# Performance work log

Measured on AMD Instinct MI355X. Metric: run time of the kernel, lower is better.

The kernel has to match this reference:

```python
import jax, jax.numpy as jnp
import numpy as np

B, S, D, H = 2, 2048, 1024, 16
HD = D // H  # head_dim = 64


def setup_inputs() -> dict:
    key = jax.random.key(0)
    ks = jax.random.split(key, 9)
    scale = 0.02
    x = jax.random.normal(ks[0], (B, S, D), dtype=jnp.float32)
    wq = jax.random.normal(ks[1], (D, D), dtype=jnp.float32) * scale
    bq = jnp.zeros((D,), dtype=jnp.float32)
    wk = jax.random.normal(ks[2], (D, D), dtype=jnp.float32) * scale
    bk = jnp.zeros((D,), dtype=jnp.float32)
    wv = jax.random.normal(ks[3], (D, D), dtype=jnp.float32) * scale
    bv = jnp.zeros((D,), dtype=jnp.float32)
    wo = jax.random.normal(ks[4], (D, D), dtype=jnp.float32) * scale
    bo = jnp.zeros((D,), dtype=jnp.float32)
    # causal mask: 1.0 where key position is in the future of query position
    mask = jnp.triu(jnp.ones((S, S), dtype=jnp.float32), k=1)[None, None]  # [1,1,S,S]
    return {"x": x, "wq": wq, "bq": bq, "wk": wk, "bk": bk,
            "wv": wv, "bv": bv, "wo": wo, "bo": bo, "mask": mask}


def reference(x, wq, bq, wk, bk, wv, bv, wo, bo, mask):
    b, s, d = x.shape
    q = (x @ wq + bq).reshape(b, s, H, HD).transpose(0, 2, 1, 3)  # [b,h,s,hd]
    k = (x @ wk + bk).reshape(b, s, H, HD).transpose(0, 2, 1, 3)
    v = (x @ wv + bv).reshape(b, s, H, HD).transpose(0, 2, 1, 3)
    scores = jnp.einsum('bhqd,bhkd->bhqk', q, k) / jnp.sqrt(jnp.float32(HD))
    scores = scores + mask * (-1e9)
    probs = jax.nn.softmax(scores, axis=-1)
    out = jnp.einsum('bhqk,bhkd->bhqd', probs, v)
    out = out.transpose(0, 2, 1, 3).reshape(b, s, d)
    return out @ wo + bo
```

## Files before the change

### kernel.cpp

```cpp
#include <hip/hip_runtime.h>
#include <hip/hip_bf16.h>
#include <cstdint>

#define DEV static __device__ __forceinline__

typedef unsigned short u16t;
typedef __attribute__((ext_vector_type(4))) float f32x4;
typedef __attribute__((ext_vector_type(4))) unsigned short u16x4;
typedef __attribute__((ext_vector_type(8))) unsigned short u16x8;
typedef __attribute__((ext_vector_type(8))) __bf16 bf16x8;

DEV u16t f2bf(float f) {
  unsigned u = __builtin_bit_cast(unsigned, f);
  u += 0x7fffu + ((u >> 16) & 1u);
  return (u16t)(u >> 16);
}
DEV float bf2f(u16t h) {
  unsigned u = ((unsigned)h) << 16;
  return __builtin_bit_cast(float, u);
}

DEV void gload_lds16(const void* g, void* l) {
  __builtin_amdgcn_global_load_lds(
      (const __attribute__((address_space(1))) void*)g,
      (__attribute__((address_space(3))) void*)l, 16, 0, 0);
}

DEV bf16x8 ldsfrag(const u16t* p) {
  return __builtin_bit_cast(bf16x8, *(const u16x8*)p);
}

DEV void bsync() {
  asm volatile("" ::: "memory");
  __builtin_amdgcn_s_barrier();
  asm volatile("" ::: "memory");
}

__global__ __launch_bounds__(256) void k_convert_x(const float* __restrict__ x,
                                                   u16t* __restrict__ xb) {
  int i = (blockIdx.x * 256 + threadIdx.x) * 4;
  f32x4 v = *(const f32x4*)&x[i];
  u16x4 o;
#pragma unroll
  for (int j = 0; j < 4; ++j) o[j] = f2bf(v[j]);
  *(u16x4*)&xb[i] = o;
}

__global__ __launch_bounds__(256) void k_transw(const float* __restrict__ w0,
                                                const float* __restrict__ w1,
                                                const float* __restrict__ w2,
                                                const float* __restrict__ w3,
                                                u16t* __restrict__ qkvT,
                                                u16t* __restrict__ oT) {
  __shared__ float lds[64][68];
  int z = blockIdx.z;
  const float* W = (z == 0) ? w0 : (z == 1) ? w1 : (z == 2) ? w2 : w3;
  u16t* OUT = (z < 3) ? (qkvT + (size_t)z * 1024 * 1024) : oT;
  int k0 = blockIdx.x * 64, n0 = blockIdx.y * 64;
  int t = threadIdx.x;
  int kl = t >> 4, n4 = (t & 15) << 2;
#pragma unroll
  for (int p = 0; p < 4; ++p) {
    f32x4 v = *(const f32x4*)&W[(size_t)(k0 + kl + p * 16) * 1024 + n0 + n4];
    *(f32x4*)&lds[kl + p * 16][n4] = v;
  }
  __syncthreads();
  int nl = t >> 4, k4 = (t & 15) << 2;
#pragma unroll
  for (int p = 0; p < 4; ++p) {
    int n = nl + p * 16;
    u16x4 o;
#pragma unroll
    for (int i = 0; i < 4; ++i) o[i] = f2bf(lds[k4 + i][n]);
    *(u16x4*)&OUT[(size_t)(n0 + n) * 1024 + k0 + k4] = o;
  }
}

template <bool BF16_OUT, bool VSPLIT>
__global__ __launch_bounds__(256) void k_gemm_bt(const u16t* __restrict__ A,
                                                 const u16t* __restrict__ BT,
                                                 void* __restrict__ Cout,
                                                 const float* __restrict__ b0,
                                                 const float* __restrict__ b1,
                                                 const float* __restrict__ b2,
                                                 u16t* __restrict__ vt,
                                                 int M, int N, int K) {
  __shared__ u16t Al[2][128 * 64];
  __shared__ u16t Bl[2][128 * 64];
  const int tid = threadIdx.x;
  const int l = tid & 63;
  const int w = tid >> 6;
  const int m0 = blockIdx.x * 128, n0 = blockIdx.y * 128;
  const int wm = (w >> 1) * 64, wn = (w & 1) * 64;
  const int lm = l & 15, lh = l >> 4;
  f32x4 acc[4][4] = {};

  auto stage = [&](int bb, int t) {
    const int k0 = t << 6;
#pragma unroll
    for (int s = 0; s < 4; ++s) {
      int c = s * 256 + tid;
      int row = c >> 3, slot = c & 7;
      int ks = k0 + (((slot ^ (row & 7)) & 7) << 3);
      gload_lds16(A + (size_t)(m0 + row) * K + ks, &Al[bb][c * 8]);
    }
#pragma unroll
    for (int s = 0; s < 4; ++s) {
      int c = s * 256 + tid;
      int row = c >> 3, slot = c & 7;
      int ks = k0 + (((slot ^ (row & 7)) & 7) << 3);
      gload_lds16(BT + (size_t)(n0 + row) * K + ks, &Bl[bb][c * 8]);
    }
  };

  const int nt = K >> 6;
  stage(0, 0);
  for (int t = 0; t < nt; ++t) {
    if (t + 1 < nt) {
      stage((t + 1) & 1, t + 1);
      asm volatile("s_waitcnt vmcnt(8)" ::: "memory");
    } else {
      asm volatile("s_waitcnt vmcnt(0)" ::: "memory");
    }
    bsync();
    const int buf = t & 1;

#pragma unroll
    for (int kk = 0; kk < 2; ++kk) {
      bf16x8 af[4], bfr[4];
#pragma unroll
      for (int i = 0; i < 4; ++i) {
        int ra = wm + i * 16 + lm;
        int sa = (kk * 4 + lh) ^ (ra & 7);
        af[i] = ldsfrag(&Al[buf][ra * 64 + sa * 8]);
        int rb = wn + i * 16 + lm;
        int sb = (kk * 4 + lh) ^ (rb & 7);
        bfr[i] = ldsfrag(&Bl[buf][rb * 64 + sb * 8]);
      }
#pragma unroll
      for (int i = 0; i < 4; ++i)
#pragma unroll
        for (int j = 0; j < 4; ++j)
          acc[i][j] = __builtin_amdgcn_mfma_f32_16x16x32_bf16(af[i], bfr[j],
                                                              acc[i][j], 0, 0, 0);
    }
    bsync();
  }

  if (!VSPLIT || (n0 + wn) < 2048) {
#pragma unroll
    for (int i = 0; i < 4; ++i) {
      int row = m0 + wm + i * 16 + (lh << 2);
#pragma unroll
      for (int j = 0; j < 4; ++j) {
        int col = n0 + wn + j * 16 + lm;
        const float* bp = (col < 1024) ? b0 : ((col < 2048) ? b1 : b2);
        float bias = bp[col & 1023];
#pragma unroll
        for (int r = 0; r < 4; ++r) {
          float v = acc[i][j][r] + bias;
          if (BF16_OUT)
            ((u16t*)Cout)[(size_t)(row + r) * N + col] = f2bf(v);
          else
            ((float*)Cout)[(size_t)(row + r) * N + col] = v;
        }
      }
    }
  } else {
#pragma unroll
    for (int i = 0; i < 4; ++i) {
      int row = m0 + wm + i * 16 + (lh << 2);
      int bidx = row >> 11, s0 = row & 2047;
#pragma unroll
    for (int j = 0; j < 4; ++j) {
        int col = n0 + wn + j * 16 + lm;
        int d = col - 2048;
        int hh = d >> 6, dd = d & 63;
        float bias = b2[d];
        u16x4 o;
#pragma unroll
        for (int r = 0; r < 4; ++r) o[r] = f2bf(acc[i][j][r] + bias);
        *(u16x4*)&vt[((size_t)((bidx * 16 + hh) * 64 + dd)) * 2048 + s0] = o;
      }
    }
  }
}

__global__ __launch_bounds__(256, 2) void k_attn(const u16t* __restrict__ qkv,
                                                 const u16t* __restrict__ vt,
                                                 u16t* __restrict__ outp) {
  __shared__ u16t Kl[2][4096];
  __shared__ u16t Vl[2][4096];
  __shared__ u16t Pl[4][2][1024];
  __shared__ u16t pad[4096];
  const int tid = threadIdx.x, l = tid & 63, w = tid >> 6;
  const int lm = l & 15, lh = l >> 4;
  const int bh = blockIdx.x, b = bh >> 4, h = bh & 15;
  const int y = blockIdx.y;
  const int qt = (y < 8) ? y : (23 - y);
  const int q0 = qt * 128;
  const int nt = 2 * qt + 2;
  const int qbase = q0 + w * 32;
  if ((size_t)qkv == 1) pad[tid] = 0;

  const u16t* Kg = qkv + (size_t)b * 2048 * 3072 + 1024 + h * 64;
  const u16t* Vg = vt + (size_t)bh * 64 * 2048;

  bf16x8 aq[2][2];
#pragma unroll
  for (int qm = 0; qm < 2; ++qm)
#pragma unroll
    for (int kk = 0; kk < 2; ++kk) {
      const u16t* src = qkv + (size_t)(b * 2048 + qbase + qm * 16 + lm) * 3072 +
                        h * 64 + kk * 32 + lh * 8;
      u16x8 v = *(const u16x8*)src;
      u16x8 o;
#pragma unroll
      for (int e = 0; e < 8; ++e) o[e] = f2bf(bf2f(v[e]) * 0.125f);
      aq[qm][kk] = __builtin_bit_cast(bf16x8, o);
    }

  float mrun[2] = {-1e30f, -1e30f};
  float lsum[2] = {0.f, 0.f};
  f32x4 aco[2][4] = {};
  const int qr0 = qbase + lm, qr1 = qbase + 16 + lm;

  auto stage = [&](int bb, int t) {
#pragma unroll
    for (int s = 0; s < 2; ++s) {
      int c = s * 256 + tid;
      int row = c >> 3, col = ((c & 7) ^ (row & 7)) << 3;
      gload_lds16(Kg + (size_t)(t * 64 + row) * 3072 + col, &Kl[bb][c * 8]);
    }
#pragma unroll
    for (int s = 0; s < 2; ++s) {
      int c = s * 256 + tid;
      int row = c >> 3, col = ((c & 7) ^ (row & 7)) << 3;
      gload_lds16(Vg + (size_t)row * 2048 + t * 64 + col, &Vl[bb][c * 8]);
    }
  };

  stage(0, 0);

  int buf = 0;
  for (int t = 0; t < nt; ++t) {
    if (t + 1 < nt) {
      stage(buf ^ 1, t + 1);
      asm volatile("s_waitcnt vmcnt(4)" ::: "memory");
    } else {
      asm volatile("s_waitcnt vmcnt(0)" ::: "memory");
    }
    bsync();

    if (t * 64 <= qbase + 31) {
      f32x4 accs[2][4] = {};
#pragma unroll
      for (int kk = 0; kk < 2; ++kk) {
        bf16x8 ak[4];
#pragma unroll
        for (int nk = 0; nk < 4; ++nk) {
          int rk = nk * 16 + lm;
          int s16 = (kk * 4 + lh) ^ (rk & 7);
          ak[nk] = ldsfrag(&Kl[buf][rk * 64 + s16 * 8]);
        }
        __builtin_amdgcn_s_setprio(1);
#pragma unroll
        for (int nk = 0; nk < 4; ++nk) {
          accs[0][nk] = __builtin_amdgcn_mfma_f32_16x16x32_bf16(
              ak[nk], aq[0][kk], accs[0][nk], 0, 0, 0);
          accs[1][nk] = __builtin_amdgcn_mfma_f32_16x16x32_bf16(
              ak[nk], aq[1][kk], accs[1][nk], 0, 0, 0);
        }
        __builtin_amdgcn_s_setprio(0);
      }

      float vmax[2] = {-1e30f, -1e30f};
      if (t * 64 + 63 > qbase) {
#pragma unroll
        for (int nk = 0; nk < 4; ++nk)
#pragma unroll
          for (int r = 0; r < 4; ++r) {
            int kvpos = t * 64 + nk * 16 + lh * 4 + r;
            float v0 = accs[0][nk][r];
            v0 = (kvpos > qr0) ? -1e30f : v0;
            accs[0][nk][r] = v0;
            vmax[0] = fmaxf(vmax[0], v0);
            float v1 = accs[1][nk][r];
            v1 = (kvpos > qr1) ? -1e30f : v1;
            accs[1][nk][r] = v1;
            vmax[1] = fmaxf(vmax[1], v1);
          }
      } else {
#pragma unroll
        for (int nk = 0; nk < 4; ++nk)
#pragma unroll
          for (int r = 0; r < 4; ++r) {
            vmax[0] = fmaxf(vmax[0], accs[0][nk][r]);
            vmax[1] = fmaxf(vmax[1], accs[1][nk][r]);
          }
      }

      if (!__all((vmax[0] <= mrun[0] + 8.f) & (vmax[1] <= mrun[1] + 8.f))) {
#pragma unroll
        for (int qm = 0; qm < 2; ++qm) {
          float rm = fmaxf(vmax[qm], __shfl_xor(vmax[qm], 16));
          rm = fmaxf(rm, __shfl_xor(rm, 32));
          float mnew = fmaxf(mrun[qm], rm);
          float alpha = __expf(mrun[qm] - mnew);
          mrun[qm] = mnew;
          lsum[qm] *= alpha;
#pragma unroll
          for (int r = 0; r < 4; ++r) {
            float ar = __shfl(alpha, lh * 4 + r);
#pragma unroll
            for (int nd = 0; nd < 4; ++nd) aco[qm][nd][r] *= ar;
          }
        }
      }

#pragma unroll
      for (int qm = 0; qm < 2; ++qm) {
        u16t* Pw = &Pl[w][qm][0];
#pragma unroll
        for (int nk = 0; nk < 4; ++nk) {
          float p0 = __expf(accs[qm][nk][0] - mrun[qm]);
          float p1 = __expf(accs[qm][nk][1] - mrun[qm]);
          float p2 = __expf(accs[qm][nk][2] - mrun[qm]);
          float p3 = __expf(accs[qm][nk][3] - mrun[qm]);
          lsum[qm] += (p0 + p1) + (p2 + p3);
          unsigned wlo, whi;
          asm("v_cvt_pk_bf16_f32 %0, %1, %2" : "=v"(wlo) : "v"(p0), "v"(p1));
          asm("v_cvt_pk_bf16_f32 %0, %1, %2" : "=v"(whi) : "v"(p2), "v"(p3));
          int off = lm * 64 + ((((2 * nk + (lh >> 1)) ^ (lm & 7)) & 7) << 3) +
                    ((lh & 1) << 2);
          *(uint2*)&Pw[off] = make_uint2(wlo, whi);
        }
      }

#pragma unroll
      for (int kk = 0; kk < 2; ++kk) {
        int sp = (kk * 4 + lh) ^ (lm & 7);
        bf16x8 ap0 = ldsfrag(&Pl[w][0][lm * 64 + sp * 8]);
        bf16x8 ap1 = ldsfrag(&Pl[w][1][lm * 64 + sp * 8]);
        __builtin_amdgcn_s_setprio(1);
#pragma unroll
        for (int nd = 0; nd < 4; ++nd) {
          int rv = nd * 16 + lm;
          int sv = (kk * 4 + lh) ^ (rv & 7);
          bf16x8 bv = ldsfrag(&Vl[buf][rv * 64 + sv * 8]);
          aco[0][nd] =
              __builtin_amdgcn_mfma_f32_16x16x32_bf16(ap0, bv, aco[0][nd], 0, 0, 0);
          aco[1][nd] =
              __builtin_amdgcn_mfma_f32_16x16x32_bf16(ap1, bv, aco[1][nd], 0, 0, 0);
        }
        __builtin_amdgcn_s_setprio(0);
      }
    }

    bsync();
    buf ^= 1;
  }

#pragma unroll
  for (int qm = 0; qm < 2; ++qm) {
    float ls = lsum[qm];
    ls += __shfl_xor(ls, 16);
    ls += __shfl_xor(ls, 32);
    float inv = 1.0f / ls;
#pragma unroll
    for (int r = 0; r < 4; ++r) {
      float ir = __shfl(inv, lh * 4 + r);
      int row = q0 + w * 32 + qm * 16 + lh * 4 + r;
#pragma unroll
      for (int nd = 0; nd < 4; ++nd) {
        int col = h * 64 + nd * 16 + lm;
        outp[(size_t)(b * 2048 + row) * 1024 + col] = f2bf(aco[qm][nd][r] * ir);
      }
    }
  }
}

extern "C" void kernel_launch(void* const* d_in, const int* in_sizes, int n_in,
                              void* d_out, int out_size, void* d_ws, size_t ws_size,
                              hipStream_t stream) {
  const float* x = (const float*)d_in[0];
  const float* wq = (const float*)d_in[1];
  const float* bq = (const float*)d_in[2];
  const float* wk = (const float*)d_in[3];
  const float* bk = (const float*)d_in[4];
  const float* wv = (const float*)d_in[5];
  const float* bv = (const float*)d_in[6];
  const float* wo = (const float*)d_in[7];
  const float* bo = (const float*)d_in[8];

  char* ws = (char*)d_ws;
  u16t* xb = (u16t*)ws;
  u16t* wqkvT = (u16t*)(ws + (8u << 20));
  u16t* woT = (u16t*)(ws + (14u << 20));
  u16t* qkv = (u16t*)(ws + (16u << 20));
  u16t* vt = (u16t*)(ws + (40u << 20));
  u16t* attn_out = xb;

  k_convert_x<<<4096, 256, 0, stream>>>(x, xb);
  k_transw<<<dim3(16, 16, 4), 256, 0, stream>>>(wq, wk, wv, wo, wqkvT, woT);
  k_gemm_bt<true, true><<<dim3(32, 24), 256, 0, stream>>>(xb, wqkvT, qkv, bq, bk,
                                                          bv, vt, 4096, 3072, 1024);
  k_attn<<<dim3(32, 16), 256, 0, stream>>>(qkv, vt, attn_out);
  k_gemm_bt<false, false><<<dim3(32, 8), 256, 0, stream>>>(
      attn_out, woT, d_out, bo, bo, bo, nullptr, 4096, 1024, 1024);
}
```

Measured before the change: 121.3 us.

## Shrink attention blocks to 64 query rows with 2 waves and exp2 softmax

Attention blocks now cover 64 query rows with two waves instead of 128 rows with four, which doubles the grid to 1024 blocks. The q-tile order is reshuffled to balance the causal workload across the grid. Because each block now only processes full or diagonal KV tiles, the per-wave skip check is removed and the mask is applied only on the last tile. The LDS padding array that limited occupancy is dropped, and the softmax switches to exp2 with log2(e) folded into the Q prescale. In exchange, each KV tile loaded into LDS is reused by fewer query rows, so total K/V traffic roughly doubles.

```diff
diff --git a/kernel.cpp b/kernel.cpp
--- a/kernel.cpp
+++ b/kernel.cpp
@@ -186,22 +186,20 @@
   }
 }
 
-__global__ __launch_bounds__(256, 2) void k_attn(const u16t* __restrict__ qkv,
+__global__ __launch_bounds__(128, 2) void k_attn(const u16t* __restrict__ qkv,
                                                  const u16t* __restrict__ vt,
                                                  u16t* __restrict__ outp) {
   __shared__ u16t Kl[2][4096];
   __shared__ u16t Vl[2][4096];
-  __shared__ u16t Pl[4][2][1024];
-  __shared__ u16t pad[4096];
+  __shared__ u16t Pl[2][2][1024];
   const int tid = threadIdx.x, l = tid & 63, w = tid >> 6;
   const int lm = l & 15, lh = l >> 4;
   const int bh = blockIdx.x, b = bh >> 4, h = bh & 15;
   const int y = blockIdx.y;
-  const int qt = (y < 8) ? y : (23 - y);
-  const int q0 = qt * 128;
-  const int nt = 2 * qt + 2;
+  const int qt = (y < 8) ? y : (y < 16) ? (39 - y) : (y < 24) ? (y - 8) : (47 - y);
+  const int q0 = qt * 64;
+  const int nt = qt + 1;
   const int qbase = q0 + w * 32;
-  if ((size_t)qkv == 1) pad[tid] = 0;
 
   const u16t* Kg = qkv + (size_t)b * 2048 * 3072 + 1024 + h * 64;
   const u16t* Vg = vt + (size_t)bh * 64 * 2048;
@@ -216,7 +214,7 @@
       u16x8 v = *(const u16x8*)src;
       u16x8 o;
 #pragma unroll
-      for (int e = 0; e < 8; ++e) o[e] = f2bf(bf2f(v[e]) * 0.125f);
+      for (int e = 0; e < 8; ++e) o[e] = f2bf(bf2f(v[e]) * 0.1803368801f);
       aq[qm][kk] = __builtin_bit_cast(bf16x8, o);
     }
 
@@ -227,14 +225,14 @@
 
   auto stage = [&](int bb, int t) {
 #pragma unroll
-    for (int s = 0; s < 2; ++s) {
-      int c = s * 256 + tid;
+    for (int s = 0; s < 4; ++s) {
+      int c = s * 128 + tid;
       int row = c >> 3, col = ((c & 7) ^ (row & 7)) << 3;
       gload_lds16(Kg + (size_t)(t * 64 + row) * 3072 + col, &Kl[bb][c * 8]);
     }
 #pragma unroll
-    for (int s = 0; s < 2; ++s) {
-      int c = s * 256 + tid;
+    for (int s = 0; s < 4; ++s) {
+      int c = s * 128 + tid;
       int row = c >> 3, col = ((c & 7) ^ (row & 7)) << 3;
       gload_lds16(Vg + (size_t)row * 2048 + t * 64 + col, &Vl[bb][c * 8]);
     }
@@ -246,115 +244,113 @@
   for (int t = 0; t < nt; ++t) {
     if (t + 1 < nt) {
       stage(buf ^ 1, t + 1);
-      asm volatile("s_waitcnt vmcnt(4)" ::: "memory");
+      asm volatile("s_waitcnt vmcnt(8)" ::: "memory");
     } else {
       asm volatile("s_waitcnt vmcnt(0)" ::: "memory");
     }
     bsync();
 
-    if (t * 64 <= qbase + 31) {
-      f32x4 accs[2][4] = {};
-#pragma unroll
-      for (int kk = 0; kk < 2; ++kk) {
-        bf16x8 ak[4];
-#pragma unroll
-        for (int nk = 0; nk < 4; ++nk) {
-          int rk = nk * 16 + lm;
-          int s16 = (kk * 4 + lh) ^ (rk & 7);
-          ak[nk] = ldsfrag(&Kl[buf][rk * 64 + s16 * 8]);
+    f32x4 accs[2][4] = {};
+#pragma unroll
+    for (int kk = 0; kk < 2; ++kk) {
+      bf16x8 ak[4];
+#pragma unroll
+      for (int nk = 0; nk < 4; ++nk) {
+        int rk = nk * 16 + lm;
+        int s16 = (kk * 4 + lh) ^ (rk & 7);
+        ak[nk] = ldsfrag(&Kl[buf][rk * 64 + s16 * 8]);
+      }
+      __builtin_amdgcn_s_setprio(1);
+#pragma unroll
+      for (int nk = 0; nk < 4; ++nk) {
+        accs[0][nk] = __builtin_amdgcn_mfma_f32_16x16x32_bf16(ak[nk], aq[0][kk],
+                                                              accs[0][nk], 0, 0, 0);
+        accs[1][nk] = __builtin_amdgcn_mfma_f32_16x16x32_bf16(ak[nk], aq[1][kk],
+                                                              accs[1][nk], 0, 0, 0);
+      }
+      __builtin_amdgcn_s_setprio(0);
+    }
+
+    float vmax[2] = {-1e30f, -1e30f};
+    if (t == nt - 1) {
+#pragma unroll
+      for (int nk = 0; nk < 4; ++nk)
+#pragma unroll
+        for (int r = 0; r < 4; ++r) {
+          int kvpos = t * 64 + nk * 16 + lh * 4 + r;
+          float v0 = accs[0][nk][r];
+          v0 = (kvpos > qr0) ? -1e30f : v0;
+          accs[0][nk][r] = v0;
+          vmax[0] = fmaxf(vmax[0], v0);
+          float v1 = accs[1][nk][r];
+          v1 = (kvpos > qr1) ? -1e30f : v1;
+          accs[1][nk][r] = v1;
+          vmax[1] = fmaxf(vmax[1], v1);
         }
-        __builtin_amdgcn_s_setprio(1);
-#pragma unroll
-        for (int nk = 0; nk < 4; ++nk) {
-          accs[0][nk] = __builtin_amdgcn_mfma_f32_16x16x32_bf16(
-              ak[nk], aq[0][kk], accs[0][nk], 0, 0, 0);
-          accs[1][nk] = __builtin_amdgcn_mfma_f32_16x16x32_bf16(
-              ak[nk], aq[1][kk], accs[1][nk], 0, 0, 0);
+    } else {
+#pragma unroll
+      for (int nk = 0; nk < 4; ++nk)
+#pragma unroll
+        for (int r = 0; r < 4; ++r) {
+          vmax[0] = fmaxf(vmax[0], accs[0][nk][r]);
+          vmax[1] = fmaxf(vmax[1], accs[1][nk][r]);
         }
-        __builtin_amdgcn_s_setprio(0);
-      }
-
-      float vmax[2] = {-1e30f, -1e30f};
-      if (t * 64 + 63 > qbase) {
-#pragma unroll
-        for (int nk = 0; nk < 4; ++nk)
-#pragma unroll
-          for (int r = 0; r < 4; ++r) {
-            int kvpos = t * 64 + nk * 16 + lh * 4 + r;
-            float v0 = accs[0][nk][r];
-            v0 = (kvpos > qr0) ? -1e30f : v0;
-            accs[0][nk][r] = v0;
-            vmax[0] = fmaxf(vmax[0], v0);
-            float v1 = accs[1][nk][r];
-            v1 = (kvpos > qr1) ? -1e30f : v1;
-            accs[1][nk][r] = v1;
-            vmax[1] = fmaxf(vmax[1], v1);
-          }
-      } else {
-#pragma unroll
-        for (int nk = 0; nk < 4; ++nk)
-#pragma unroll
-          for (int r = 0; r < 4; ++r) {
-            vmax[0] = fmaxf(vmax[0], accs[0][nk][r]);
-            vmax[1] = fmaxf(vmax[1], accs[1][nk][r]);
-          }
-      }
-
-      if (!__all((vmax[0] <= mrun[0] + 8.f) & (vmax[1] <= mrun[1] + 8.f))) {
-#pragma unroll
-        for (int qm = 0; qm < 2; ++qm) {
-          float rm = fmaxf(vmax[qm], __shfl_xor(vmax[qm], 16));
-          rm = fmaxf(rm, __shfl_xor(rm, 32));
-          float mnew = fmaxf(mrun[qm], rm);
-          float alpha = __expf(mrun[qm] - mnew);
-          mrun[qm] = mnew;
-          lsum[qm] *= alpha;
-#pragma unroll
-          for (int r = 0; r < 4; ++r) {
-            float ar = __shfl(alpha, lh * 4 + r);
-#pragma unroll
-            for (int nd = 0; nd < 4; ++nd) aco[qm][nd][r] *= ar;
-          }
+    }
+
+    if (!__all((vmax[0] <= mrun[0] + 8.f) & (vmax[1] <= mrun[1] + 8.f))) {
+#pragma unroll
+      for (int qm = 0; qm < 2; ++qm) {
+        float rm = fmaxf(vmax[qm], __shfl_xor(vmax[qm], 16));
+        rm = fmaxf(rm, __shfl_xor(rm, 32));
+        float mnew = fmaxf(mrun[qm], rm);
+        float alpha = exp2f(mrun[qm] - mnew);
+        mrun[qm] = mnew;
+        lsum[qm] *= alpha;
+#pragma unroll
+        for (int r = 0; r < 4; ++r) {
+          float ar = __shfl(alpha, lh * 4 + r);
+#pragma unroll
+          for (int nd = 0; nd < 4; ++nd) aco[qm][nd][r] *= ar;
         }
       }
-
-#pragma unroll
-      for (int qm = 0; qm < 2; ++qm) {
-        u16t* Pw = &Pl[w][qm][0];
-#pragma unroll
-        for (int nk = 0; nk < 4; ++nk) {
-          float p0 = __expf(accs[qm][nk][0] - mrun[qm]);
-          float p1 = __expf(accs[qm][nk][1] - mrun[qm]);
-          float p2 = __expf(accs[qm][nk][2] - mrun[qm]);
-          float p3 = __expf(accs[qm][nk][3] - mrun[qm]);
-          lsum[qm] += (p0 + p1) + (p2 + p3);
-          unsigned wlo, whi;
-          asm("v_cvt_pk_bf16_f32 %0, %1, %2" : "=v"(wlo) : "v"(p0), "v"(p1));
-          asm("v_cvt_pk_bf16_f32 %0, %1, %2" : "=v"(whi) : "v"(p2), "v"(p3));
-          int off = lm * 64 + ((((2 * nk + (lh >> 1)) ^ (lm & 7)) & 7) << 3) +
-                    ((lh & 1) << 2);
-          *(uint2*)&Pw[off] = make_uint2(wlo, whi);
-        }
-      }
-
-#pragma unroll
-      for (int kk = 0; kk < 2; ++kk) {
-        int sp = (kk * 4 + lh) ^ (lm & 7);
-        bf16x8 ap0 = ldsfrag(&Pl[w][0][lm * 64 + sp * 8]);
-        bf16x8 ap1 = ldsfrag(&Pl[w][1][lm * 64 + sp * 8]);
-        __builtin_amdgcn_s_setprio(1);
-#pragma unroll
-        for (int nd = 0; nd < 4; ++nd) {
-          int rv = nd * 16 + lm;
-          int sv = (kk * 4 + lh) ^ (rv & 7);
-          bf16x8 bv = ldsfrag(&Vl[buf][rv * 64 + sv * 8]);
-          aco[0][nd] =
-              __builtin_amdgcn_mfma_f32_16x16x32_bf16(ap0, bv, aco[0][nd], 0, 0, 0);
-          aco[1][nd] =
-              __builtin_amdgcn_mfma_f32_16x16x32_bf16(ap1, bv, aco[1][nd], 0, 0, 0);
-        }
-        __builtin_amdgcn_s_setprio(0);
-      }
+    }
+
+#pragma unroll
+    for (int qm = 0; qm < 2; ++qm) {
+      u16t* Pw = &Pl[w][qm][0];
+#pragma unroll
+      for (int nk = 0; nk < 4; ++nk) {
+        float p0 = exp2f(accs[qm][nk][0] - mrun[qm]);
+        float p1 = exp2f(accs[qm][nk][1] - mrun[qm]);
+        float p2 = exp2f(accs[qm][nk][2] - mrun[qm]);
+        float p3 = exp2f(accs[qm][nk][3] - mrun[qm]);
+        lsum[qm] += (p0 + p1) + (p2 + p3);
+        unsigned wlo, whi;
+        asm("v_cvt_pk_bf16_f32 %0, %1, %2" : "=v"(wlo) : "v"(p0), "v"(p1));
+        asm("v_cvt_pk_bf16_f32 %0, %1, %2" : "=v"(whi) : "v"(p2), "v"(p3));
+        int off = lm * 64 + ((((2 * nk + (lh >> 1)) ^ (lm & 7)) & 7) << 3) +
+                  ((lh & 1) << 2);
+        *(uint2*)&Pw[off] = make_uint2(wlo, whi);
+      }
+    }
+
+#pragma unroll
+    for (int kk = 0; kk < 2; ++kk) {
+      int sp = (kk * 4 + lh) ^ (lm & 7);
+      bf16x8 ap0 = ldsfrag(&Pl[w][0][lm * 64 + sp * 8]);
+      bf16x8 ap1 = ldsfrag(&Pl[w][1][lm * 64 + sp * 8]);
+      __builtin_amdgcn_s_setprio(1);
+#pragma unroll
+      for (int nd = 0; nd < 4; ++nd) {
+        int rv = nd * 16 + lm;
+        int sv = (kk * 4 + lh) ^ (rv & 7);
+        bf16x8 bv = ldsfrag(&Vl[buf][rv * 64 + sv * 8]);
+        aco[0][nd] =
+            __builtin_amdgcn_mfma_f32_16x16x32_bf16(ap0, bv, aco[0][nd], 0, 0, 0);
+        aco[1][nd] =
+            __builtin_amdgcn_mfma_f32_16x16x32_bf16(ap1, bv, aco[1][nd], 0, 0, 0);
+      }
+      __builtin_amdgcn_s_setprio(0);
     }
 
     bsync();
@@ -370,7 +366,7 @@
 #pragma unroll
     for (int r = 0; r < 4; ++r) {
       float ir = __shfl(inv, lh * 4 + r);
-      int row = q0 + w * 32 + qm * 16 + lh * 4 + r;
+      int row = qbase + qm * 16 + lh * 4 + r;
 #pragma unroll
       for (int nd = 0; nd < 4; ++nd) {
         int col = h * 64 + nd * 16 + lm;
@@ -405,7 +401,7 @@
   k_transw<<<dim3(16, 16, 4), 256, 0, stream>>>(wq, wk, wv, wo, wqkvT, woT);
   k_gemm_bt<true, true><<<dim3(32, 24), 256, 0, stream>>>(xb, wqkvT, qkv, bq, bk,
                                                           bv, vt, 4096, 3072, 1024);
-  k_attn<<<dim3(32, 16), 256, 0, stream>>>(qkv, vt, attn_out);
+  k_attn<<<dim3(32, 32), 128, 0, stream>>>(qkv, vt, attn_out);
   k_gemm_bt<false, false><<<dim3(32, 8), 256, 0, stream>>>(
       attn_out, woT, d_out, bo, bo, bo, nullptr, 4096, 1024, 1024);
 }
```

New measurement: 131.4 us. 8.3% more time.
